# Optimization experiments

Measured on AMD Instinct MI355X. Metric: run time of the kernel, lower is better.

## Reference

```python
import jax, jax.numpy as jnp
import numpy as np

B, S, D = 4, 2048, 1024


def setup_inputs() -> dict:
    key = jax.random.key(0)
    ks = jax.random.split(key, 9)
    scale = 1.0 / np.sqrt(D)
    x = jax.random.normal(ks[0], (B, S, D), dtype=jnp.float32)
    mask = jnp.tril(jnp.ones((S, S), dtype=jnp.int32))[None, :, :]  # causal, broadcast over batch
    Wq = jax.random.normal(ks[1], (D, D), dtype=jnp.float32) * scale
    bq = jax.random.normal(ks[2], (D,), dtype=jnp.float32) * 0.01
    Wk = jax.random.normal(ks[3], (D, D), dtype=jnp.float32) * scale
    bk = jax.random.normal(ks[4], (D,), dtype=jnp.float32) * 0.01
    Wv = jax.random.normal(ks[5], (D, D), dtype=jnp.float32) * scale
    bv = jax.random.normal(ks[6], (D,), dtype=jnp.float32) * 0.01
    Wo = jax.random.normal(ks[7], (D, D), dtype=jnp.float32) * scale
    bo = jax.random.normal(ks[8], (D,), dtype=jnp.float32) * 0.01
    return {"x": x, "mask": mask, "Wq": Wq, "bq": bq, "Wk": Wk, "bk": bk,
            "Wv": Wv, "bv": bv, "Wo": Wo, "bo": bo}


def reference(x, mask, Wq, bq, Wk, bk, Wv, bv, Wo, bo):
    # Linear projections (torch Linear: x @ W^T + b; here W stored as [in, out])
    Q = jnp.einsum('bsd,de->bse', x, Wq) + bq
    K = jnp.einsum('bsd,de->bse', x, Wk) + bk
    V = jnp.einsum('bsd,de->bse', x, Wv) + bv
    d_k = Q.shape[-1]
    scores = jnp.einsum('bqd,bkd->bqk', Q, K) / jnp.sqrt(jnp.float32(d_k))
    scores = jnp.where(mask == 0, jnp.float32(-jnp.inf), scores)
    attn_weights = jax.nn.softmax(scores, axis=-1)  # [B, S, S]
    attn_output = jnp.einsum('bqk,bkd->bqd', attn_weights, V)
    output = jnp.einsum('bsd,de->bse', attn_output, Wo) + bo
    return output, attn_weights
```

## Files before the change

kernel.cpp:

```cpp
#include <hip/hip_runtime.h>
#include <cstdint>
#include <cstddef>
#include <cmath>

typedef __bf16 bf16_t;
typedef bf16_t bf16x8 __attribute__((ext_vector_type(8)));
typedef bf16_t bf16x4 __attribute__((ext_vector_type(4)));
typedef float f32x4 __attribute__((ext_vector_type(4)));

constexpr int kB = 4;
constexpr int kS = 2048;
constexpr int kD = 1024;
constexpr int BM = 128, BN = 128, BK = 32;
constexpr int TILE_ELEMS = (BM + BN) * BK;

typedef __attribute__((address_space(1))) void as1void;
typedef __attribute__((address_space(3))) void as3void;

__device__ __forceinline__ void gload16(const void* g, void* l) {
  __builtin_amdgcn_global_load_lds((as1void*)g, (as3void*)l, 16, 0, 0);
}

__device__ __forceinline__ void gemm_mainloop(
    const bf16_t* __restrict__ A, int lda,
    const bf16_t* __restrict__ B, int ldb,
    int ksteps, bf16_t* lds, f32x4 acc[4][4]) {
  const int tid = threadIdx.x;
  const int w = tid >> 6, lane = tid & 63;
  const int srow = lane >> 2;
  const int scol = (lane & 3) << 3;
  const int wr = (w >> 1) << 6, wc = (w & 1) << 6;
  const int fr = lane & 15, kg = lane >> 4;

  const bf16_t* ga0 = A + (size_t)(w * 16 + srow) * lda + scol;
  const bf16_t* ga1 = A + (size_t)(64 + w * 16 + srow) * lda + scol;
  const bf16_t* gb0 = B + (size_t)(w * 16 + srow) * ldb + scol;
  const bf16_t* gb1 = B + (size_t)(64 + w * 16 + srow) * ldb + scol;
  const int oa0 = (w * 16) * BK;
  const int oa1 = (64 + w * 16) * BK;
  const int ob0 = BM * BK + (w * 16) * BK;
  const int ob1 = BM * BK + (64 + w * 16) * BK;

  gload16(ga0, lds + oa0);
  gload16(ga1, lds + oa1);
  gload16(gb0, lds + ob0);
  gload16(gb1, lds + ob1);
  ga0 += BK; ga1 += BK; gb0 += BK; gb1 += BK;
  __syncthreads();

  int cur = 0;
  for (int ks = 0; ks < ksteps; ++ks) {
    const int nxt = cur ^ 1;
    if (ks + 1 < ksteps) {
      bf16_t* nb = lds + nxt * TILE_ELEMS;
      gload16(ga0, nb + oa0);
      gload16(ga1, nb + oa1);
      gload16(gb0, nb + ob0);
      gload16(gb1, nb + ob1);
      ga0 += BK; ga1 += BK; gb0 += BK; gb1 += BK;
    }
    const bf16_t* cb = lds + cur * TILE_ELEMS;
    bf16x8 af[4], bfv[4];
#pragma unroll
    for (int m = 0; m < 4; ++m)
      af[m] = *(const bf16x8*)(cb + (wr + m * 16 + fr) * BK + kg * 8);
#pragma unroll
    for (int n = 0; n < 4; ++n)
      bfv[n] = *(const bf16x8*)(cb + BM * BK + (wc + n * 16 + fr) * BK + kg * 8);
#pragma unroll
    for (int m = 0; m < 4; ++m)
#pragma unroll
      for (int n = 0; n < 4; ++n)
        acc[m][n] = __builtin_amdgcn_mfma_f32_16x16x32_bf16(af[m], bfv[n],
                                                            acc[m][n], 0, 0, 0);
    __syncthreads();
    cur = nxt;
  }
}


__global__ __launch_bounds__(256)
void k_gemm_qkv(const bf16_t* __restrict__ A, const bf16_t* __restrict__ WT,
                const float* __restrict__ bq, const float* __restrict__ bk,
                const float* __restrict__ bv, bf16_t* __restrict__ Out) {
  __shared__ bf16_t lds[2 * TILE_ELEMS];
  const int which = blockIdx.x >> 3;
  const int n0 = (blockIdx.x & 7) * BN;
  const int m0 = blockIdx.y * BM;
  f32x4 acc[4][4] = {};
  gemm_mainloop(A + (size_t)m0 * kD, kD,
                WT + (size_t)which * kD * kD + (size_t)n0 * kD, kD,
                kD / BK, lds, acc);
  const float* bias = which == 0 ? bq : which == 1 ? bk : bv;
  const int tid = threadIdx.x, w = tid >> 6, lane = tid & 63;
  const int wr = (w >> 1) << 6, wc = (w & 1) << 6, fr = lane & 15, kg = lane >> 4;
  if (which < 2) {
    bf16_t* C = Out + (size_t)which * kB * kS * kD;
#pragma unroll
    for (int n = 0; n < 4; ++n) {
      const int col = n0 + wc + n * 16 + fr;
      const float bvv = bias[col];
#pragma unroll
      for (int m = 0; m < 4; ++m)
#pragma unroll
        for (int i = 0; i < 4; ++i) {
          const int row = m0 + wr + m * 16 + kg * 4 + i;
          C[(size_t)row * kD + col] = (bf16_t)(acc[m][n][i] + bvv);
        }
    }
  } else {
    bf16_t* VT = Out + (size_t)2 * kB * kS * kD;
#pragma unroll
    for (int n = 0; n < 4; ++n) {
      const int col = n0 + wc + n * 16 + fr;
      const float bvv = bias[col];
#pragma unroll
      for (int m = 0; m < 4; ++m)
#pragma unroll
        for (int i = 0; i < 4; ++i) {
          const int row = m0 + wr + m * 16 + kg * 4 + i;
          const int b = row >> 11, s = row & (kS - 1);
          VT[((size_t)b * kD + col) * kS + s] = (bf16_t)(acc[m][n][i] + bvv);
        }
    }
  }
}

__global__ __launch_bounds__(256)
void k_gemm_scores(const bf16_t* __restrict__ Q, const bf16_t* __restrict__ K,
                   float* __restrict__ Sc) {
  const int t = blockIdx.x, b = blockIdx.y;
  int by = (int)((sqrtf(8.f * t + 1.f) - 1.f) * 0.5f);
  while ((by + 1) * (by + 2) / 2 <= t) ++by;
  while (by * (by + 1) / 2 > t) --by;
  const int bx = t - by * (by + 1) / 2;
  __shared__ bf16_t lds[2 * TILE_ELEMS];
  const int m0 = by * BM, n0 = bx * BN;
  f32x4 acc[4][4] = {};
  gemm_mainloop(Q + (size_t)b * kS * kD + (size_t)m0 * kD, kD,
                K + (size_t)b * kS * kD + (size_t)n0 * kD, kD, kD / BK, lds, acc);
  float* Sb = Sc + (size_t)b * kS * kS;
  const int tid = threadIdx.x, w = tid >> 6, lane = tid & 63;
  const int wr = (w >> 1) << 6, wc = (w & 1) << 6, fr = lane & 15, kg = lane >> 4;
#pragma unroll
  for (int m = 0; m < 4; ++m)
#pragma unroll
    for (int n = 0; n < 4; ++n)
#pragma unroll
      for (int i = 0; i < 4; ++i) {
        const int row = m0 + wr + m * 16 + kg * 4 + i;
        const int col = n0 + wc + n * 16 + fr;
        Sb[(size_t)row * kS + col] = acc[m][n][i] * 0.03125f;
      }
}

__global__ __launch_bounds__(256)
void k_softmax(float* __restrict__ P, bf16_t* __restrict__ Pb) {
  const int row = blockIdx.x;
  const int q = row & (kS - 1);
  float* p = P + (size_t)row * kS;
  bf16_t* pb = Pb + (size_t)row * kS;
  const int L = q + 1;
  __shared__ float buf[kS];
  __shared__ float red[8];
  const int tid = threadIdx.x;
  float4* b4 = (float4*)buf;
  const float4* p4 = (const float4*)p;
  b4[tid] = p4[tid];
  b4[tid + 256] = p4[tid + 256];
  __syncthreads();
  float mx = -1e30f;
  for (int k = tid; k < L; k += 256) mx = fmaxf(mx, buf[k]);
#pragma unroll
  for (int s2 = 32; s2 >= 1; s2 >>= 1) mx = fmaxf(mx, __shfl_xor(mx, s2));
  if ((tid & 63) == 0) red[tid >> 6] = mx;
  __syncthreads();
  mx = fmaxf(fmaxf(red[0], red[1]), fmaxf(red[2], red[3]));
  float sm = 0.f;
  for (int k = tid; k < L; k += 256) {
    const float e = __expf(buf[k] - mx);
    buf[k] = e;
    sm += e;
  }
#pragma unroll
  for (int s2 = 32; s2 >= 1; s2 >>= 1) sm += __shfl_xor(sm, s2);
  if ((tid & 63) == 0) red[4 + (tid >> 6)] = sm;
  __syncthreads();
  const float inv = 1.f / (red[4] + red[5] + red[6] + red[7]);
  for (int k = tid; k < L; k += 256) {
    const float v = buf[k] * inv;
    p[k] = v;
    pb[k] = (bf16_t)v;
  }
  for (int k = L + tid; k < kS; k += 256) {
    p[k] = 0.f;
    pb[k] = (bf16_t)0.f;
  }
}

__global__ __launch_bounds__(256)
void k_gemm_pv(const bf16_t* __restrict__ P, const bf16_t* __restrict__ VT,
               bf16_t* __restrict__ AO) {
  const int bx = blockIdx.x, b = blockIdx.z;
  const int by = (int)gridDim.y - 1 - (int)blockIdx.y;
  __shared__ bf16_t lds[2 * TILE_ELEMS];
  const int m0 = by * BM, n0 = bx * BN;
  const int ksteps = (m0 + BM) / BK;
  f32x4 acc[4][4] = {};
  gemm_mainloop(P + (size_t)b * kS * kS + (size_t)m0 * kS, kS,
                VT + (size_t)b * kD * kS + (size_t)n0 * kS, kS, ksteps, lds, acc);
  bf16_t* AOb = AO + (size_t)b * kS * kD;
  const int tid = threadIdx.x, w = tid >> 6, lane = tid & 63;
  const int wr = (w >> 1) << 6, wc = (w & 1) << 6, fr = lane & 15, kg = lane >> 4;
#pragma unroll
  for (int m = 0; m < 4; ++m)
#pragma unroll
    for (int n = 0; n < 4; ++n)
#pragma unroll
      for (int i = 0; i < 4; ++i) {
        const int row = m0 + wr + m * 16 + kg * 4 + i;
        const int col = n0 + wc + n * 16 + fr;
        AOb[(size_t)row * kD + col] = (bf16_t)acc[m][n][i];
      }
}

__global__ __launch_bounds__(256)
void k_gemm_out(const bf16_t* __restrict__ A, const bf16_t* __restrict__ Bw,
                const float* __restrict__ bias, float* __restrict__ C) {
  __shared__ bf16_t lds[2 * TILE_ELEMS];
  const int m0 = blockIdx.y * BM, n0 = blockIdx.x * BN;
  f32x4 acc[4][4] = {};
  gemm_mainloop(A + (size_t)m0 * kD, kD, Bw + (size_t)n0 * kD, kD, kD / BK, lds, acc);
  const int tid = threadIdx.x, w = tid >> 6, lane = tid & 63;
  const int wr = (w >> 1) << 6, wc = (w & 1) << 6, fr = lane & 15, kg = lane >> 4;
#pragma unroll
  for (int n = 0; n < 4; ++n) {
    const int col = n0 + wc + n * 16 + fr;
    const float bv = bias[col];
#pragma unroll
    for (int m = 0; m < 4; ++m)
#pragma unroll
      for (int i = 0; i < 4; ++i) {
        const int row = m0 + wr + m * 16 + kg * 4 + i;
        C[(size_t)row * kD + col] = acc[m][n][i] + bv;
      }
  }
}

__global__ __launch_bounds__(256)
void k_cvt(const float* __restrict__ X, bf16_t* __restrict__ Y, size_t n4) {
  size_t i = (size_t)blockIdx.x * 256 + threadIdx.x;
  const size_t stride = (size_t)gridDim.x * 256;
  const float4* X4 = (const float4*)X;
  bf16x4* Y4 = (bf16x4*)Y;
  for (; i < n4; i += stride) {
    const float4 v = X4[i];
    bf16x4 o = {(bf16_t)v.x, (bf16_t)v.y, (bf16_t)v.z, (bf16_t)v.w};
    Y4[i] = o;
  }
}

__global__ __launch_bounds__(256)
void k_prep_w(const float* __restrict__ W0, const float* __restrict__ W1,
              const float* __restrict__ W2, const float* __restrict__ W3,
              bf16_t* __restrict__ T0, bf16_t* __restrict__ T1,
              bf16_t* __restrict__ T2, bf16_t* __restrict__ T3) {
  const float* W = blockIdx.z == 0 ? W0 : blockIdx.z == 1 ? W1 : blockIdx.z == 2 ? W2 : W3;
  bf16_t* T = blockIdx.z == 0 ? T0 : blockIdx.z == 1 ? T1 : blockIdx.z == 2 ? T2 : T3;
  __shared__ float t[32][33];
  const int tx = threadIdx.x, ty = threadIdx.y;
  const int x0 = blockIdx.x * 32, y0 = blockIdx.y * 32;
#pragma unroll
  for (int j = 0; j < 4; ++j)
    t[ty + 8 * j][tx] = W[(size_t)(y0 + ty + 8 * j) * kD + x0 + tx];
  __syncthreads();
#pragma unroll
  for (int j = 0; j < 4; ++j)
    T[(size_t)(x0 + ty + 8 * j) * kD + y0 + tx] = (bf16_t)t[tx][ty + 8 * j];
}

extern "C" void kernel_launch(void* const* d_in, const int* in_sizes, int n_in,
                              void* d_out, int out_size, void* d_ws, size_t ws_size,
                              hipStream_t stream) {
  (void)in_sizes; (void)n_in; (void)out_size; (void)ws_size;
  const float* x  = (const float*)d_in[0];
  const float* Wq = (const float*)d_in[2];
  const float* bq = (const float*)d_in[3];
  const float* Wk = (const float*)d_in[4];
  const float* bk = (const float*)d_in[5];
  const float* Wv = (const float*)d_in[6];
  const float* bv = (const float*)d_in[7];
  const float* Wo = (const float*)d_in[8];
  const float* bo = (const float*)d_in[9];

  float* out  = (float*)d_out;
  float* Pout = out + (size_t)kB * kS * kD;

  bf16_t* WqT = (bf16_t*)d_ws;
  bf16_t* WkT = WqT + (size_t)kD * kD;
  bf16_t* WvT = WkT + (size_t)kD * kD;
  bf16_t* WoT = WvT + (size_t)kD * kD;
  bf16_t* Qb  = WoT + (size_t)kD * kD;
  bf16_t* Kb  = Qb + (size_t)kB * kS * kD;
  bf16_t* VTb = Kb + (size_t)kB * kS * kD;
  bf16_t* Pb  = VTb + (size_t)kB * kS * kD;
  bf16_t* AOb = Pb + (size_t)kB * kS * kS;
  bf16_t* xb  = AOb + (size_t)kB * kS * kD;

  k_cvt<<<2048, 256, 0, stream>>>(x, xb, (size_t)kB * kS * kD / 4);
  k_prep_w<<<dim3(32, 32, 4), dim3(32, 8), 0, stream>>>(Wq, Wk, Wv, Wo, WqT, WkT, WvT, WoT);
  k_gemm_qkv<<<dim3(24, kB * kS / BM), 256, 0, stream>>>(xb, WqT, bq, bk, bv, Qb);
  k_gemm_scores<<<dim3(136, kB), 256, 0, stream>>>(Qb, Kb, Pout);
  k_softmax<<<kB * kS, 256, 0, stream>>>(Pout, Pb);
  k_gemm_pv<<<dim3(kD / BN, kS / BM, kB), 256, 0, stream>>>(Pb, VTb, AOb);
  k_gemm_out<<<dim3(kD / BN, kB * kS / BM), 256, 0, stream>>>(AOb, WoT, bo, out);
}
```

Before: 232.1 us.

## Template GEMM mainloop with fragment-ordered LDS layout, larger QKV tiles and swizzled grids

Replaces the shared GEMM mainloop with a templated version whose LDS tile layout is stored in MFMA fragment order (16-row groups by k-chunk), which aims to cut LDS bank conflicts on fragment reads. The QKV projection moves to 256x128 tiles with 512 threads, and the QKV and output GEMMs get block-index swizzles for better L2 reuse. The input conversion and weight transpose kernels are merged into one launch, occupancy hints are added, and softmax skips loading masked-out score chunks. Together these aim to raise MFMA throughput and trim launch and memory overhead. The cost is higher register and LDS pressure per block.

Result: slower. 273.1 us (+17.7%).

```diff
diff --git a/kernel.cpp b/kernel.cpp
--- a/kernel.cpp
+++ b/kernel.cpp
@@ -11,8 +11,6 @@
 constexpr int kB = 4;
 constexpr int kS = 2048;
 constexpr int kD = 1024;
-constexpr int BM = 128, BN = 128, BK = 32;
-constexpr int TILE_ELEMS = (BM + BN) * BK;
 
 typedef __attribute__((address_space(1))) void as1void;
 typedef __attribute__((address_space(3))) void as3void;
@@ -21,90 +19,102 @@
   __builtin_amdgcn_global_load_lds((as1void*)g, (as3void*)l, 16, 0, 0);
 }
 
-__device__ __forceinline__ void gemm_mainloop(
+template <int TM, int TN, int NTHR>
+__device__ __forceinline__ void gemm2ph(
     const bf16_t* __restrict__ A, int lda,
     const bf16_t* __restrict__ B, int ldb,
-    int ksteps, bf16_t* lds, f32x4 acc[4][4]) {
+    int nk, bf16_t* lds, f32x4 acc[4][4]) {
+  constexpr int WND = TN / 64;
+  constexpr int IA = TM * 4 / NTHR;
+  constexpr int IB = TN * 4 / NTHR;
+  constexpr int BUF = (TM + TN) * 32;
   const int tid = threadIdx.x;
-  const int w = tid >> 6, lane = tid & 63;
-  const int srow = lane >> 2;
-  const int scol = (lane & 3) << 3;
-  const int wr = (w >> 1) << 6, wc = (w & 1) << 6;
+  const int wid = tid >> 6, lane = tid & 63;
+  const int wm = wid / WND, wn = wid % WND;
   const int fr = lane & 15, kg = lane >> 4;
 
-  const bf16_t* ga0 = A + (size_t)(w * 16 + srow) * lda + scol;
-  const bf16_t* ga1 = A + (size_t)(64 + w * 16 + srow) * lda + scol;
-  const bf16_t* gb0 = B + (size_t)(w * 16 + srow) * ldb + scol;
-  const bf16_t* gb1 = B + (size_t)(64 + w * 16 + srow) * ldb + scol;
-  const int oa0 = (w * 16) * BK;
-  const int oa1 = (64 + w * 16) * BK;
-  const int ob0 = BM * BK + (w * 16) * BK;
-  const int ob1 = BM * BK + (64 + w * 16) * BK;
-
-  gload16(ga0, lds + oa0);
-  gload16(ga1, lds + oa1);
-  gload16(gb0, lds + ob0);
-  gload16(gb1, lds + ob1);
-  ga0 += BK; ga1 += BK; gb0 += BK; gb1 += BK;
+  const bf16_t* gA[IA]; int oA[IA];
+#pragma unroll
+  for (int i = 0; i < IA; ++i) {
+    const int u = tid + i * NTHR;
+    const int r = ((u >> 6) << 4) | (u & 15);
+    const int c = ((u >> 4) & 3) << 3;
+    gA[i] = A + (size_t)r * lda + c;
+    oA[i] = u * 8;
+  }
+  const bf16_t* gB[IB]; int oB[IB];
+#pragma unroll
+  for (int i = 0; i < IB; ++i) {
+    const int u = tid + i * NTHR;
+    const int r = ((u >> 6) << 4) | (u & 15);
+    const int c = ((u >> 4) & 3) << 3;
+    gB[i] = B + (size_t)r * ldb + c;
+    oB[i] = TM * 32 + u * 8;
+  }
+#pragma unroll
+  for (int i = 0; i < IA; ++i) gload16(gA[i], lds + oA[i]);
+#pragma unroll
+  for (int i = 0; i < IB; ++i) gload16(gB[i], lds + oB[i]);
   __syncthreads();
 
   int cur = 0;
-  for (int ks = 0; ks < ksteps; ++ks) {
-    const int nxt = cur ^ 1;
-    if (ks + 1 < ksteps) {
-      bf16_t* nb = lds + nxt * TILE_ELEMS;
-      gload16(ga0, nb + oa0);
-      gload16(ga1, nb + oa1);
-      gload16(gb0, nb + ob0);
-      gload16(gb1, nb + ob1);
-      ga0 += BK; ga1 += BK; gb0 += BK; gb1 += BK;
+  const int aoff = kg * 128 + fr * 8;
+  for (int t = 0; t < nk; ++t) {
+    if (t + 1 < nk) {
+      bf16_t* nb = lds + (cur ^ 1) * BUF;
+#pragma unroll
+      for (int i = 0; i < IA; ++i) gload16(gA[i] + (t + 1) * 32, nb + oA[i]);
+#pragma unroll
+      for (int i = 0; i < IB; ++i) gload16(gB[i] + (t + 1) * 32, nb + oB[i]);
     }
-    const bf16_t* cb = lds + cur * TILE_ELEMS;
-    bf16x8 af[4], bfv[4];
-#pragma unroll
-    for (int m = 0; m < 4; ++m)
-      af[m] = *(const bf16x8*)(cb + (wr + m * 16 + fr) * BK + kg * 8);
+    const bf16_t* cb = lds + cur * BUF;
+    bf16x8 aF[4], bF[4];
+#pragma unroll
+    for (int m = 0; m < 4; ++m)
+      aF[m] = *(const bf16x8*)(cb + (wm * 4 + m) * 512 + aoff);
 #pragma unroll
     for (int n = 0; n < 4; ++n)
-      bfv[n] = *(const bf16x8*)(cb + BM * BK + (wc + n * 16 + fr) * BK + kg * 8);
+      bF[n] = *(const bf16x8*)(cb + TM * 32 + (wn * 4 + n) * 512 + aoff);
 #pragma unroll
     for (int m = 0; m < 4; ++m)
 #pragma unroll
       for (int n = 0; n < 4; ++n)
-        acc[m][n] = __builtin_amdgcn_mfma_f32_16x16x32_bf16(af[m], bfv[n],
+        acc[m][n] = __builtin_amdgcn_mfma_f32_16x16x32_bf16(aF[m], bF[n],
                                                             acc[m][n], 0, 0, 0);
     __syncthreads();
-    cur = nxt;
-  }
-}
-
-
-__global__ __launch_bounds__(256)
-void k_gemm_qkv(const bf16_t* __restrict__ A, const bf16_t* __restrict__ WT,
-                const float* __restrict__ bq, const float* __restrict__ bk,
-                const float* __restrict__ bv, bf16_t* __restrict__ Out) {
-  __shared__ bf16_t lds[2 * TILE_ELEMS];
-  const int which = blockIdx.x >> 3;
-  const int n0 = (blockIdx.x & 7) * BN;
-  const int m0 = blockIdx.y * BM;
+    cur ^= 1;
+  }
+}
+
+
+__global__ __launch_bounds__(512, 4)
+void k_qkv(const bf16_t* __restrict__ A, const bf16_t* __restrict__ WT,
+           const float* __restrict__ bq, const float* __restrict__ bk,
+           const float* __restrict__ bv, bf16_t* __restrict__ Out) {
+  __shared__ bf16_t lds[2 * (256 + 128) * 32];
+  const int id = blockIdx.x;
+  const int swz = (id & 7) * 96 + (id >> 3);
+  const int mb = swz / 24, nbb = swz % 24;
+  const int which = nbb >> 3;
+  const int m0 = mb * 256, n0 = (nbb & 7) * 128;
   f32x4 acc[4][4] = {};
-  gemm_mainloop(A + (size_t)m0 * kD, kD,
-                WT + (size_t)which * kD * kD + (size_t)n0 * kD, kD,
-                kD / BK, lds, acc);
+  gemm2ph<256, 128, 512>(A + (size_t)m0 * kD, kD,
+                         WT + (size_t)which * kD * kD + (size_t)n0 * kD, kD,
+                         kD / 32, lds, acc);
   const float* bias = which == 0 ? bq : which == 1 ? bk : bv;
-  const int tid = threadIdx.x, w = tid >> 6, lane = tid & 63;
-  const int wr = (w >> 1) << 6, wc = (w & 1) << 6, fr = lane & 15, kg = lane >> 4;
+  const int lane = threadIdx.x & 63, wid = threadIdx.x >> 6;
+  const int wm = wid >> 1, wn = wid & 1, fr = lane & 15, kgr = lane >> 4;
   if (which < 2) {
     bf16_t* C = Out + (size_t)which * kB * kS * kD;
 #pragma unroll
     for (int n = 0; n < 4; ++n) {
-      const int col = n0 + wc + n * 16 + fr;
+      const int col = n0 + wn * 64 + n * 16 + fr;
       const float bvv = bias[col];
 #pragma unroll
       for (int m = 0; m < 4; ++m)
 #pragma unroll
         for (int i = 0; i < 4; ++i) {
-          const int row = m0 + wr + m * 16 + kg * 4 + i;
+          const int row = m0 + wm * 64 + m * 16 + kgr * 4 + i;
           C[(size_t)row * kD + col] = (bf16_t)(acc[m][n][i] + bvv);
         }
     }
@@ -112,13 +122,13 @@
     bf16_t* VT = Out + (size_t)2 * kB * kS * kD;
 #pragma unroll
     for (int n = 0; n < 4; ++n) {
-      const int col = n0 + wc + n * 16 + fr;
+      const int col = n0 + wn * 64 + n * 16 + fr;
       const float bvv = bias[col];
 #pragma unroll
       for (int m = 0; m < 4; ++m)
 #pragma unroll
         for (int i = 0; i < 4; ++i) {
-          const int row = m0 + wr + m * 16 + kg * 4 + i;
+          const int row = m0 + wm * 64 + m * 16 + kgr * 4 + i;
           const int b = row >> 11, s = row & (kS - 1);
           VT[((size_t)b * kD + col) * kS + s] = (bf16_t)(acc[m][n][i] + bvv);
         }
@@ -126,32 +136,88 @@
   }
 }
 
-__global__ __launch_bounds__(256)
-void k_gemm_scores(const bf16_t* __restrict__ Q, const bf16_t* __restrict__ K,
-                   float* __restrict__ Sc) {
+__global__ __launch_bounds__(256, 4)
+void k_scores(const bf16_t* __restrict__ Q, const bf16_t* __restrict__ K,
+              float* __restrict__ Sc) {
   const int t = blockIdx.x, b = blockIdx.y;
   int by = (int)((sqrtf(8.f * t + 1.f) - 1.f) * 0.5f);
   while ((by + 1) * (by + 2) / 2 <= t) ++by;
   while (by * (by + 1) / 2 > t) --by;
   const int bx = t - by * (by + 1) / 2;
-  __shared__ bf16_t lds[2 * TILE_ELEMS];
-  const int m0 = by * BM, n0 = bx * BN;
+  __shared__ bf16_t lds[2 * 256 * 32];
+  const int m0 = by * 128, n0 = bx * 128;
   f32x4 acc[4][4] = {};
-  gemm_mainloop(Q + (size_t)b * kS * kD + (size_t)m0 * kD, kD,
-                K + (size_t)b * kS * kD + (size_t)n0 * kD, kD, kD / BK, lds, acc);
+  gemm2ph<128, 128, 256>(Q + (size_t)b * kS * kD + (size_t)m0 * kD, kD,
+                         K + (size_t)b * kS * kD + (size_t)n0 * kD, kD,
+                         kD / 32, lds, acc);
   float* Sb = Sc + (size_t)b * kS * kS;
-  const int tid = threadIdx.x, w = tid >> 6, lane = tid & 63;
-  const int wr = (w >> 1) << 6, wc = (w & 1) << 6, fr = lane & 15, kg = lane >> 4;
-#pragma unroll
-  for (int m = 0; m < 4; ++m)
-#pragma unroll
-    for (int n = 0; n < 4; ++n)
+  const int lane = threadIdx.x & 63, wid = threadIdx.x >> 6;
+  const int wm = wid >> 1, wn = wid & 1, fr = lane & 15, kgr = lane >> 4;
+#pragma unroll
+  for (int n = 0; n < 4; ++n) {
+    const int col = n0 + wn * 64 + n * 16 + fr;
+#pragma unroll
+    for (int m = 0; m < 4; ++m)
 #pragma unroll
       for (int i = 0; i < 4; ++i) {
-        const int row = m0 + wr + m * 16 + kg * 4 + i;
-        const int col = n0 + wc + n * 16 + fr;
+        const int row = m0 + wm * 64 + m * 16 + kgr * 4 + i;
         Sb[(size_t)row * kS + col] = acc[m][n][i] * 0.03125f;
       }
+  }
+}
+
+__global__ __launch_bounds__(256, 4)
+void k_pv(const bf16_t* __restrict__ P, const bf16_t* __restrict__ VT,
+          bf16_t* __restrict__ AO) {
+  const int bx = blockIdx.x, b = blockIdx.z;
+  const int by = (int)gridDim.y - 1 - (int)blockIdx.y;
+  __shared__ bf16_t lds[2 * 256 * 32];
+  const int m0 = by * 128, n0 = bx * 128;
+  const int nk = (m0 + 128) / 32;
+  f32x4 acc[4][4] = {};
+  gemm2ph<128, 128, 256>(P + (size_t)b * kS * kS + (size_t)m0 * kS, kS,
+                         VT + (size_t)b * kD * kS + (size_t)n0 * kS, kS,
+                         nk, lds, acc);
+  bf16_t* AOb = AO + (size_t)b * kS * kD;
+  const int lane = threadIdx.x & 63, wid = threadIdx.x >> 6;
+  const int wm = wid >> 1, wn = wid & 1, fr = lane & 15, kgr = lane >> 4;
+#pragma unroll
+  for (int n = 0; n < 4; ++n) {
+    const int col = n0 + wn * 64 + n * 16 + fr;
+#pragma unroll
+    for (int m = 0; m < 4; ++m)
+#pragma unroll
+      for (int i = 0; i < 4; ++i) {
+        const int row = m0 + wm * 64 + m * 16 + kgr * 4 + i;
+        AOb[(size_t)row * kD + col] = (bf16_t)acc[m][n][i];
+      }
+  }
+}
+
+__global__ __launch_bounds__(256, 4)
+void k_out(const bf16_t* __restrict__ A, const bf16_t* __restrict__ Bw,
+           const float* __restrict__ bias, float* __restrict__ C) {
+  __shared__ bf16_t lds[2 * 256 * 32];
+  const int id = blockIdx.x;
+  const int swz = (id & 7) * 64 + (id >> 3);
+  const int m0 = (swz >> 3) * 128, n0 = (swz & 7) * 128;
+  f32x4 acc[4][4] = {};
+  gemm2ph<128, 128, 256>(A + (size_t)m0 * kD, kD, Bw + (size_t)n0 * kD, kD,
+                         kD / 32, lds, acc);
+  const int lane = threadIdx.x & 63, wid = threadIdx.x >> 6;
+  const int wm = wid >> 1, wn = wid & 1, fr = lane & 15, kgr = lane >> 4;
+#pragma unroll
+  for (int n = 0; n < 4; ++n) {
+    const int col = n0 + wn * 64 + n * 16 + fr;
+    const float bvv = bias[col];
+#pragma unroll
+    for (int m = 0; m < 4; ++m)
+#pragma unroll
+      for (int i = 0; i < 4; ++i) {
+        const int row = m0 + wm * 64 + m * 16 + kgr * 4 + i;
+        C[(size_t)row * kD + col] = acc[m][n][i] + bvv;
+      }
+  }
 }
 
 __global__ __launch_bounds__(256)
@@ -166,8 +232,8 @@
   const int tid = threadIdx.x;
   float4* b4 = (float4*)buf;
   const float4* p4 = (const float4*)p;
-  b4[tid] = p4[tid];
-  b4[tid + 256] = p4[tid + 256];
+  if (tid * 4 < L) b4[tid] = p4[tid];
+  if (1024 + tid * 4 < L) b4[tid + 256] = p4[tid + 256];
   __syncthreads();
   float mx = -1e30f;
   for (int k = tid; k < L; k += 256) mx = fmaxf(mx, buf[k]);
@@ -199,76 +265,28 @@
 }
 
 __global__ __launch_bounds__(256)
-void k_gemm_pv(const bf16_t* __restrict__ P, const bf16_t* __restrict__ VT,
-               bf16_t* __restrict__ AO) {
-  const int bx = blockIdx.x, b = blockIdx.z;
-  const int by = (int)gridDim.y - 1 - (int)blockIdx.y;
-  __shared__ bf16_t lds[2 * TILE_ELEMS];
-  const int m0 = by * BM, n0 = bx * BN;
-  const int ksteps = (m0 + BM) / BK;
-  f32x4 acc[4][4] = {};
-  gemm_mainloop(P + (size_t)b * kS * kS + (size_t)m0 * kS, kS,
-                VT + (size_t)b * kD * kS + (size_t)n0 * kS, kS, ksteps, lds, acc);
-  bf16_t* AOb = AO + (size_t)b * kS * kD;
-  const int tid = threadIdx.x, w = tid >> 6, lane = tid & 63;
-  const int wr = (w >> 1) << 6, wc = (w & 1) << 6, fr = lane & 15, kg = lane >> 4;
-#pragma unroll
-  for (int m = 0; m < 4; ++m)
-#pragma unroll
-    for (int n = 0; n < 4; ++n)
-#pragma unroll
-      for (int i = 0; i < 4; ++i) {
-        const int row = m0 + wr + m * 16 + kg * 4 + i;
-        const int col = n0 + wc + n * 16 + fr;
-        AOb[(size_t)row * kD + col] = (bf16_t)acc[m][n][i];
-      }
-}
-
-__global__ __launch_bounds__(256)
-void k_gemm_out(const bf16_t* __restrict__ A, const bf16_t* __restrict__ Bw,
-                const float* __restrict__ bias, float* __restrict__ C) {
-  __shared__ bf16_t lds[2 * TILE_ELEMS];
-  const int m0 = blockIdx.y * BM, n0 = blockIdx.x * BN;
-  f32x4 acc[4][4] = {};
-  gemm_mainloop(A + (size_t)m0 * kD, kD, Bw + (size_t)n0 * kD, kD, kD / BK, lds, acc);
-  const int tid = threadIdx.x, w = tid >> 6, lane = tid & 63;
-  const int wr = (w >> 1) << 6, wc = (w & 1) << 6, fr = lane & 15, kg = lane >> 4;
-#pragma unroll
-  for (int n = 0; n < 4; ++n) {
-    const int col = n0 + wc + n * 16 + fr;
-    const float bv = bias[col];
-#pragma unroll
-    for (int m = 0; m < 4; ++m)
-#pragma unroll
-      for (int i = 0; i < 4; ++i) {
-        const int row = m0 + wr + m * 16 + kg * 4 + i;
-        C[(size_t)row * kD + col] = acc[m][n][i] + bv;
-      }
-  }
-}
-
-__global__ __launch_bounds__(256)
-void k_cvt(const float* __restrict__ X, bf16_t* __restrict__ Y, size_t n4) {
-  size_t i = (size_t)blockIdx.x * 256 + threadIdx.x;
-  const size_t stride = (size_t)gridDim.x * 256;
-  const float4* X4 = (const float4*)X;
-  bf16x4* Y4 = (bf16x4*)Y;
-  for (; i < n4; i += stride) {
-    const float4 v = X4[i];
-    bf16x4 o = {(bf16_t)v.x, (bf16_t)v.y, (bf16_t)v.z, (bf16_t)v.w};
-    Y4[i] = o;
-  }
-}
-
-__global__ __launch_bounds__(256)
-void k_prep_w(const float* __restrict__ W0, const float* __restrict__ W1,
-              const float* __restrict__ W2, const float* __restrict__ W3,
-              bf16_t* __restrict__ T0, bf16_t* __restrict__ T1,
-              bf16_t* __restrict__ T2, bf16_t* __restrict__ T3) {
+void k_prep(const float* __restrict__ X, bf16_t* __restrict__ Y,
+            const float* __restrict__ W0, const float* __restrict__ W1,
+            const float* __restrict__ W2, const float* __restrict__ W3,
+            bf16_t* __restrict__ T0, bf16_t* __restrict__ T1,
+            bf16_t* __restrict__ T2, bf16_t* __restrict__ T3) {
+  const int tx = threadIdx.x & 31, ty = threadIdx.x >> 5;
+  if (blockIdx.z == 4) {
+    const size_t n4 = (size_t)kB * kS * kD / 4;
+    size_t i = ((size_t)blockIdx.y * 32 + blockIdx.x) * 256 + threadIdx.x;
+    const size_t stride = (size_t)1024 * 256;
+    const float4* X4 = (const float4*)X;
+    bf16x4* Y4 = (bf16x4*)Y;
+    for (; i < n4; i += stride) {
+      const float4 v = X4[i];
+      bf16x4 o = {(bf16_t)v.x, (bf16_t)v.y, (bf16_t)v.z, (bf16_t)v.w};
+      Y4[i] = o;
+    }
+    return;
+  }
   const float* W = blockIdx.z == 0 ? W0 : blockIdx.z == 1 ? W1 : blockIdx.z == 2 ? W2 : W3;
   bf16_t* T = blockIdx.z == 0 ? T0 : blockIdx.z == 1 ? T1 : blockIdx.z == 2 ? T2 : T3;
   __shared__ float t[32][33];
-  const int tx = threadIdx.x, ty = threadIdx.y;
   const int x0 = blockIdx.x * 32, y0 = blockIdx.y * 32;
 #pragma unroll
   for (int j = 0; j < 4; ++j)
@@ -307,11 +325,11 @@
   bf16_t* AOb = Pb + (size_t)kB * kS * kS;
   bf16_t* xb  = AOb + (size_t)kB * kS * kD;
 
-  k_cvt<<<2048, 256, 0, stream>>>(x, xb, (size_t)kB * kS * kD / 4);
-  k_prep_w<<<dim3(32, 32, 4), dim3(32, 8), 0, stream>>>(Wq, Wk, Wv, Wo, WqT, WkT, WvT, WoT);
-  k_gemm_qkv<<<dim3(24, kB * kS / BM), 256, 0, stream>>>(xb, WqT, bq, bk, bv, Qb);
-  k_gemm_scores<<<dim3(136, kB), 256, 0, stream>>>(Qb, Kb, Pout);
+  k_prep<<<dim3(32, 32, 5), 256, 0, stream>>>(x, xb, Wq, Wk, Wv, Wo,
+                                              WqT, WkT, WvT, WoT);
+  k_qkv<<<768, 512, 0, stream>>>(xb, WqT, bq, bk, bv, Qb);
+  k_scores<<<dim3(136, kB), 256, 0, stream>>>(Qb, Kb, Pout);
   k_softmax<<<kB * kS, 256, 0, stream>>>(Pout, Pb);
-  k_gemm_pv<<<dim3(kD / BN, kS / BM, kB), 256, 0, stream>>>(Pb, VTb, AOb);
-  k_gemm_out<<<dim3(kD / BN, kB * kS / BM), 256, 0, stream>>>(AOb, WoT, bo, out);
-}
+  k_pv<<<dim3(8, 16, kB), 256, 0, stream>>>(Pb, VTb, AOb);
+  k_out<<<512, 256, 0, stream>>>(AOb, WoT, bo, out);
+}
```

## Use 8-wave phased pipelined QKV GEMM, fuse prep kernels, trim softmax loads

Applied to the files above, without the earlier changes.

Replaces the QKV projection GEMM with a 512-thread, 128x256-tile kernel. Each K-step is split into four phases, with global-to-LDS loads interleaved between MFMA groups, explicit waitcnt and barriers, s_setprio around the MFMAs, and a swizzled block ordering. It also merges the x conversion and weight transpose into one launch, and makes softmax skip loading fully masked float4 chunks of each row. The hand-scheduled pipeline aims to hide load latency and reduce launch overhead, at the cost of fragile manual synchronisation and higher LDS use per block.

Result: no change. 234.2 us (+0.9%).

```diff
diff --git a/kernel.cpp b/kernel.cpp
--- a/kernel.cpp
+++ b/kernel.cpp
@@ -19,6 +19,12 @@
 
 __device__ __forceinline__ void gload16(const void* g, void* l) {
   __builtin_amdgcn_global_load_lds((as1void*)g, (as3void*)l, 16, 0, 0);
+}
+
+__device__ __forceinline__ void wgbar() {
+  asm volatile("" ::: "memory");
+  __builtin_amdgcn_s_barrier();
+  asm volatile("" ::: "memory");
 }
 
 __device__ __forceinline__ void gemm_mainloop(
@@ -78,33 +84,137 @@
   }
 }
 
-
-__global__ __launch_bounds__(256)
-void k_gemm_qkv(const bf16_t* __restrict__ A, const bf16_t* __restrict__ WT,
-                const float* __restrict__ bq, const float* __restrict__ bk,
-                const float* __restrict__ bv, bf16_t* __restrict__ Out) {
-  __shared__ bf16_t lds[2 * TILE_ELEMS];
-  const int which = blockIdx.x >> 3;
-  const int n0 = (blockIdx.x & 7) * BN;
-  const int m0 = blockIdx.y * BM;
+__device__ __forceinline__ void gemm8ph(
+    const bf16_t* __restrict__ A, int lda,
+    const bf16_t* __restrict__ B, int ldb,
+    int nk, bf16_t* lds, f32x4 acc[4][4]) {
+  const int tid = threadIdx.x;
+  const int wid = tid >> 6, lane = tid & 63;
+  const int wm = wid >> 2, wn = wid & 3;
+  const int fr = lane & 15, kg = (lane >> 4) & 3;
+  const int srow = ((tid >> 7) << 4) | (tid & 15);
+  const int scol = ((tid >> 4) & 7) << 3;
+  const bf16_t* pA = A + (size_t)srow * lda + scol;
+  const bf16_t* pB = B + (size_t)srow * ldb + scol;
+  const int dst = tid * 8;
+
+  auto stgA = [&](int t, int j) {
+    gload16(pA + (size_t)(j * 64) * lda + t * 64,
+            lds + (t & 1) * 24576 + j * 4096 + dst);
+  };
+  auto stgB = [&](int t, int j) {
+    gload16(pB + (size_t)(j * 64) * ldb + t * 64,
+            lds + (t & 1) * 24576 + 8192 + j * 4096 + dst);
+  };
+
+  stgB(0, 0); stgB(0, 1); stgB(0, 2); stgB(0, 3);
+  stgA(0, 0); stgA(0, 1);
+  if (nk > 1) {
+    stgB(1, 0); stgB(1, 1); stgB(1, 2); stgB(1, 3);
+    asm volatile("s_waitcnt vmcnt(4)" ::: "memory");
+  } else {
+    asm volatile("s_waitcnt vmcnt(0)" ::: "memory");
+  }
+  wgbar();
+
+  const int ro = kg * 128 + fr * 8;
+  for (int t = 0; t < nk; ++t) {
+    const bf16_t* bb = lds + (t & 1) * 24576;
+    const bf16_t* as = bb + wm * 4096;
+    const bf16_t* bs = bb + 8192 + wn * 4096;
+    bf16x8 bF[4][2], aF[2];
+#pragma unroll
+    for (int n = 0; n < 4; ++n) {
+      bF[n][0] = *(const bf16x8*)(bs + n * 1024 + ro);
+      bF[n][1] = *(const bf16x8*)(bs + n * 1024 + 512 + ro);
+    }
+    aF[0] = *(const bf16x8*)(as + ro);
+    aF[1] = *(const bf16x8*)(as + 512 + ro);
+    if (t + 1 < nk) { stgA(t + 1, 0); stgA(t + 1, 1); }
+    wgbar();
+    __builtin_amdgcn_s_setprio(1);
+#pragma unroll
+    for (int n = 0; n < 4; ++n) {
+      acc[0][n] = __builtin_amdgcn_mfma_f32_16x16x32_bf16(aF[0], bF[n][0], acc[0][n], 0, 0, 0);
+      acc[0][n] = __builtin_amdgcn_mfma_f32_16x16x32_bf16(aF[1], bF[n][1], acc[0][n], 0, 0, 0);
+    }
+    __builtin_amdgcn_s_setprio(0);
+    asm volatile("s_waitcnt lgkmcnt(0)" ::: "memory");
+    wgbar();
+    aF[0] = *(const bf16x8*)(as + 1024 + ro);
+    aF[1] = *(const bf16x8*)(as + 1024 + 512 + ro);
+    if (t + 2 < nk) { stgB(t + 2, 0); stgB(t + 2, 1); }
+    wgbar();
+    __builtin_amdgcn_s_setprio(1);
+#pragma unroll
+    for (int n = 0; n < 4; ++n) {
+      acc[1][n] = __builtin_amdgcn_mfma_f32_16x16x32_bf16(aF[0], bF[n][0], acc[1][n], 0, 0, 0);
+      acc[1][n] = __builtin_amdgcn_mfma_f32_16x16x32_bf16(aF[1], bF[n][1], acc[1][n], 0, 0, 0);
+    }
+    __builtin_amdgcn_s_setprio(0);
+    asm volatile("s_waitcnt lgkmcnt(0)" ::: "memory");
+    wgbar();
+    aF[0] = *(const bf16x8*)(as + 2048 + ro);
+    aF[1] = *(const bf16x8*)(as + 2048 + 512 + ro);
+    if (t + 2 < nk) { stgB(t + 2, 2); stgB(t + 2, 3); }
+    wgbar();
+    __builtin_amdgcn_s_setprio(1);
+#pragma unroll
+    for (int n = 0; n < 4; ++n) {
+      acc[2][n] = __builtin_amdgcn_mfma_f32_16x16x32_bf16(aF[0], bF[n][0], acc[2][n], 0, 0, 0);
+      acc[2][n] = __builtin_amdgcn_mfma_f32_16x16x32_bf16(aF[1], bF[n][1], acc[2][n], 0, 0, 0);
+    }
+    __builtin_amdgcn_s_setprio(0);
+    asm volatile("s_waitcnt lgkmcnt(0)" ::: "memory");
+    wgbar();
+    aF[0] = *(const bf16x8*)(as + 3072 + ro);
+    aF[1] = *(const bf16x8*)(as + 3072 + 512 + ro);
+    wgbar();
+    __builtin_amdgcn_s_setprio(1);
+#pragma unroll
+    for (int n = 0; n < 4; ++n) {
+      acc[3][n] = __builtin_amdgcn_mfma_f32_16x16x32_bf16(aF[0], bF[n][0], acc[3][n], 0, 0, 0);
+      acc[3][n] = __builtin_amdgcn_mfma_f32_16x16x32_bf16(aF[1], bF[n][1], acc[3][n], 0, 0, 0);
+    }
+    __builtin_amdgcn_s_setprio(0);
+    asm volatile("s_waitcnt lgkmcnt(0)" ::: "memory");
+    if (t < nk - 1) {
+      if (t + 2 < nk) asm volatile("s_waitcnt vmcnt(4)" ::: "memory");
+      else            asm volatile("s_waitcnt vmcnt(0)" ::: "memory");
+    }
+    wgbar();
+  }
+}
+
+
+__global__ __launch_bounds__(512)
+void k_qkv8(const bf16_t* __restrict__ A, const bf16_t* __restrict__ WT,
+            const float* __restrict__ bq, const float* __restrict__ bk,
+            const float* __restrict__ bv, bf16_t* __restrict__ Out) {
+  __shared__ bf16_t lds[49152];
+  const int id = blockIdx.x;
+  const int swz = (id & 7) * 96 + (id >> 3);
+  const int mb = swz / 12, nb = swz % 12;
+  const int which = nb >> 2;
+  const int m0 = mb * 128, n0 = (nb & 3) * 256;
   f32x4 acc[4][4] = {};
-  gemm_mainloop(A + (size_t)m0 * kD, kD,
-                WT + (size_t)which * kD * kD + (size_t)n0 * kD, kD,
-                kD / BK, lds, acc);
+  gemm8ph(A + (size_t)m0 * kD, kD,
+          WT + (size_t)which * kD * kD + (size_t)n0 * kD, kD,
+          kD / 64, lds, acc);
   const float* bias = which == 0 ? bq : which == 1 ? bk : bv;
-  const int tid = threadIdx.x, w = tid >> 6, lane = tid & 63;
-  const int wr = (w >> 1) << 6, wc = (w & 1) << 6, fr = lane & 15, kg = lane >> 4;
+  const int lane = threadIdx.x & 63, wid = threadIdx.x >> 6;
+  const int wm = wid >> 2, wn = wid & 3, fr = lane & 15, kgr = lane >> 4;
   if (which < 2) {
     bf16_t* C = Out + (size_t)which * kB * kS * kD;
 #pragma unroll
     for (int n = 0; n < 4; ++n) {
-      const int col = n0 + wc + n * 16 + fr;
+      const int col = n0 + wn * 64 + n * 16 + fr;
       const float bvv = bias[col];
 #pragma unroll
       for (int m = 0; m < 4; ++m)
 #pragma unroll
         for (int i = 0; i < 4; ++i) {
-          const int row = m0 + wr + m * 16 + kg * 4 + i;
+          const int row = m0 + wm * 64 + m * 16 + kgr * 4 + i;
           C[(size_t)row * kD + col] = (bf16_t)(acc[m][n][i] + bvv);
         }
     }
@@ -112,13 +222,13 @@
     bf16_t* VT = Out + (size_t)2 * kB * kS * kD;
 #pragma unroll
     for (int n = 0; n < 4; ++n) {
-      const int col = n0 + wc + n * 16 + fr;
+      const int col = n0 + wn * 64 + n * 16 + fr;
       const float bvv = bias[col];
 #pragma unroll
       for (int m = 0; m < 4; ++m)
 #pragma unroll
         for (int i = 0; i < 4; ++i) {
-          const int row = m0 + wr + m * 16 + kg * 4 + i;
+          const int row = m0 + wm * 64 + m * 16 + kgr * 4 + i;
           const int b = row >> 11, s = row & (kS - 1);
           VT[((size_t)b * kD + col) * kS + s] = (bf16_t)(acc[m][n][i] + bvv);
         }
@@ -166,8 +276,8 @@
   const int tid = threadIdx.x;
   float4* b4 = (float4*)buf;
   const float4* p4 = (const float4*)p;
-  b4[tid] = p4[tid];
-  b4[tid + 256] = p4[tid + 256];
+  if (tid * 4 < L) b4[tid] = p4[tid];
+  if (1024 + tid * 4 < L) b4[tid + 256] = p4[tid + 256];
   __syncthreads();
   float mx = -1e30f;
   for (int k = tid; k < L; k += 256) mx = fmaxf(mx, buf[k]);
@@ -248,27 +358,28 @@
 }
 
 __global__ __launch_bounds__(256)
-void k_cvt(const float* __restrict__ X, bf16_t* __restrict__ Y, size_t n4) {
-  size_t i = (size_t)blockIdx.x * 256 + threadIdx.x;
-  const size_t stride = (size_t)gridDim.x * 256;
-  const float4* X4 = (const float4*)X;
-  bf16x4* Y4 = (bf16x4*)Y;
-  for (; i < n4; i += stride) {
-    const float4 v = X4[i];
-    bf16x4 o = {(bf16_t)v.x, (bf16_t)v.y, (bf16_t)v.z, (bf16_t)v.w};
-    Y4[i] = o;
-  }
-}
-
-__global__ __launch_bounds__(256)
-void k_prep_w(const float* __restrict__ W0, const float* __restrict__ W1,
-              const float* __restrict__ W2, const float* __restrict__ W3,
-              bf16_t* __restrict__ T0, bf16_t* __restrict__ T1,
-              bf16_t* __restrict__ T2, bf16_t* __restrict__ T3) {
+void k_prep(const float* __restrict__ X, bf16_t* __restrict__ Y,
+            const float* __restrict__ W0, const float* __restrict__ W1,
+            const float* __restrict__ W2, const float* __restrict__ W3,
+            bf16_t* __restrict__ T0, bf16_t* __restrict__ T1,
+            bf16_t* __restrict__ T2, bf16_t* __restrict__ T3) {
+  const int tx = threadIdx.x & 31, ty = threadIdx.x >> 5;
+  if (blockIdx.z == 4) {
+    const size_t n4 = (size_t)kB * kS * kD / 4;
+    size_t i = ((size_t)blockIdx.y * 32 + blockIdx.x) * 256 + threadIdx.x;
+    const size_t stride = (size_t)1024 * 256;
+    const float4* X4 = (const float4*)X;
+    bf16x4* Y4 = (bf16x4*)Y;
+    for (; i < n4; i += stride) {
+      const float4 v = X4[i];
+      bf16x4 o = {(bf16_t)v.x, (bf16_t)v.y, (bf16_t)v.z, (bf16_t)v.w};
+      Y4[i] = o;
+    }
+    return;
+  }
   const float* W = blockIdx.z == 0 ? W0 : blockIdx.z == 1 ? W1 : blockIdx.z == 2 ? W2 : W3;
   bf16_t* T = blockIdx.z == 0 ? T0 : blockIdx.z == 1 ? T1 : blockIdx.z == 2 ? T2 : T3;
   __shared__ float t[32][33];
-  const int tx = threadIdx.x, ty = threadIdx.y;
   const int x0 = blockIdx.x * 32, y0 = blockIdx.y * 32;
 #pragma unroll
   for (int j = 0; j < 4; ++j)
@@ -307,11 +418,11 @@
   bf16_t* AOb = Pb + (size_t)kB * kS * kS;
   bf16_t* xb  = AOb + (size_t)kB * kS * kD;
 
-  k_cvt<<<2048, 256, 0, stream>>>(x, xb, (size_t)kB * kS * kD / 4);
-  k_prep_w<<<dim3(32, 32, 4), dim3(32, 8), 0, stream>>>(Wq, Wk, Wv, Wo, WqT, WkT, WvT, WoT);
-  k_gemm_qkv<<<dim3(24, kB * kS / BM), 256, 0, stream>>>(xb, WqT, bq, bk, bv, Qb);
+  k_prep<<<dim3(32, 32, 5), 256, 0, stream>>>(x, xb, Wq, Wk, Wv, Wo,
+                                              WqT, WkT, WvT, WoT);
+  k_qkv8<<<768, 512, 0, stream>>>(xb, WqT, bq, bk, bv, Qb);
   k_gemm_scores<<<dim3(136, kB), 256, 0, stream>>>(Qb, Kb, Pout);
   k_softmax<<<kB * kS, 256, 0, stream>>>(Pout, Pb);
-  k_gemm_pv<<<dim3(kD / BN, kS / BM, kB), 256, 0, stream>>>(Pb, VTb, AOb);
-  k_gemm_out<<<dim3(kD / BN, kB * kS / BM), 256, 0, stream>>>(AOb, WoT, bo, out);
-}
+  k_gemm_pv<<<dim3(8, 16, kB), 256, 0, stream>>>(Pb, VTb, AOb);
+  k_gemm_out<<<dim3(8, 64), 256, 0, stream>>>(AOb, WoT, bo, out);
+}
```

## Add 256x256 ping-pong GEMM for Q/K projection, fuse prep kernels, swizzle tiles

Applied to the files above, without the earlier changes.

Splits the QKV projection into a new 512-thread 256x256-tile GEMM for Q and K, with a multi-stage global-to-LDS pipeline, interleaved staging, raw barriers and setprio. V keeps the 128-tile path and moves to its own kernel. It also fuses the x conversion and weight transpose into one launch, adds block-index swizzling to the V and output GEMMs, and makes softmax load only the causal prefix of each row. The aim is higher MFMA utilisation and better L2 reuse, at the cost of heavier register and LDS pressure and fragile hand-written waitcnt logic.

New measurement: 220.9 us. 1.05x faster.

```diff
diff --git a/kernel.cpp b/kernel.cpp
--- a/kernel.cpp
+++ b/kernel.cpp
@@ -19,6 +19,12 @@
 
 __device__ __forceinline__ void gload16(const void* g, void* l) {
   __builtin_amdgcn_global_load_lds((as1void*)g, (as3void*)l, 16, 0, 0);
+}
+
+__device__ __forceinline__ void wgbar() {
+  asm volatile("" ::: "memory");
+  __builtin_amdgcn_s_barrier();
+  asm volatile("" ::: "memory");
 }
 
 __device__ __forceinline__ void gemm_mainloop(
@@ -78,51 +84,137 @@
   }
 }
 
-
-__global__ __launch_bounds__(256)
-void k_gemm_qkv(const bf16_t* __restrict__ A, const bf16_t* __restrict__ WT,
-                const float* __restrict__ bq, const float* __restrict__ bk,
-                const float* __restrict__ bv, bf16_t* __restrict__ Out) {
+__device__ __forceinline__ void gemm256_loop(
+    const bf16_t* __restrict__ A, int lda,
+    const bf16_t* __restrict__ B, int ldb,
+    int nk, bf16_t* lds, f32x4 acc[8][4]) {
+  const int tid = threadIdx.x;
+  const int wid = tid >> 6, lane = tid & 63;
+  const int wm = wid >> 2, wn = wid & 3;
+  const int fr = lane & 15, kg = (lane >> 4) & 3;
+  const int s_row = ((tid >> 7) << 4) | (tid & 15);
+  const int s_col = ((tid >> 4) & 7) << 3;
+  const bf16_t* pA = A + (size_t)s_row * lda + s_col;
+  const bf16_t* pB = B + (size_t)s_row * ldb + s_col;
+  const int ldst = wid << 9;
+
+  auto stg = [&](int tt, int op, int h, int j) {
+    const bf16_t* g = (op ? pB : pA) + (size_t)(h * 128 + j * 64) * (op ? ldb : lda)
+                      + (size_t)tt * 64;
+    bf16_t* d = lds + (((tt & 1) * 4 + op * 2 + h) * 8192) + j * 4096 + ldst;
+    gload16(g, d);
+  };
+
+#pragma unroll
+  for (int h = 0; h < 2; ++h)
+#pragma unroll
+    for (int j = 0; j < 2; ++j) { stg(0, 0, h, j); stg(0, 1, h, j); }
+  stg(1, 1, 0, 0); stg(1, 1, 0, 1); stg(1, 1, 1, 0); stg(1, 1, 1, 1);
+  stg(1, 0, 0, 0); stg(1, 0, 1, 0);
+  asm volatile("s_waitcnt vmcnt(6)" ::: "memory");
+  wgbar();
+
+  const int arow = kg * 128 + fr * 8;
+  for (int t = 0; t < nk; ++t) {
+    const bf16_t* sb = lds + (t & 1) * 32768;
+    const bf16_t* aslot = sb + wm * 8192;
+    const bf16_t* bslot = sb + (2 + (wn >> 1)) * 8192 + (wn & 1) * 4096;
+    bf16x8 bF[4][2];
+#pragma unroll
+    for (int q = 0; q < 4; ++q) {
+      bf16x8 aF[2][2];
+#pragma unroll
+      for (int mi = 0; mi < 2; ++mi)
+#pragma unroll
+        for (int ks = 0; ks < 2; ++ks)
+          aF[mi][ks] = *(const bf16x8*)(aslot + (2 * q + mi) * 1024 + ks * 512 + arow);
+      if (q == 0) {
+#pragma unroll
+        for (int n = 0; n < 4; ++n)
+#pragma unroll
+          for (int ks = 0; ks < 2; ++ks)
+            bF[n][ks] = *(const bf16x8*)(bslot + n * 1024 + ks * 512 + arow);
+      }
+      if (q == 0)      { if (t + 1 <= nk - 1) { stg(t + 1, 0, 0, 1); stg(t + 1, 0, 1, 1); } }
+      else if (q == 1) { if (t + 2 <= nk - 1) { stg(t + 2, 1, 0, 0); stg(t + 2, 1, 0, 1); } }
+      else if (q == 2) { if (t + 2 <= nk - 1) { stg(t + 2, 1, 1, 0); stg(t + 2, 1, 1, 1); } }
+      else             { if (t + 2 <= nk - 1) { stg(t + 2, 0, 0, 0); stg(t + 2, 0, 1, 0); } }
+      wgbar();
+      __builtin_amdgcn_s_setprio(1);
+#pragma unroll
+      for (int mi = 0; mi < 2; ++mi)
+#pragma unroll
+        for (int n = 0; n < 4; ++n)
+#pragma unroll
+          for (int ks = 0; ks < 2; ++ks)
+            acc[2 * q + mi][n] = __builtin_amdgcn_mfma_f32_16x16x32_bf16(
+                aF[mi][ks], bF[n][ks], acc[2 * q + mi][n], 0, 0, 0);
+      __builtin_amdgcn_s_setprio(0);
+      asm volatile("s_waitcnt lgkmcnt(0)" ::: "memory");
+      if (q == 3 && t < nk - 1) {
+        if (t + 2 <= nk - 1) asm volatile("s_waitcnt vmcnt(6)" ::: "memory");
+        else                 asm volatile("s_waitcnt vmcnt(0)" ::: "memory");
+      }
+      wgbar();
+    }
+  }
+}
+
+
+__global__ __launch_bounds__(512, 2)
+void k_qk256(const bf16_t* __restrict__ A, const bf16_t* __restrict__ WT,
+             const float* __restrict__ bq, const float* __restrict__ bk,
+             bf16_t* __restrict__ Qb, bf16_t* __restrict__ Kb) {
+  __shared__ bf16_t lds[65536];
+  const int id = blockIdx.x;
+  const int swz = (id & 7) * 32 + (id >> 3);
+  const int mb = swz >> 3, nb = swz & 7;
+  const int m0 = mb * 256, n0 = nb * 256;
+  f32x4 acc[8][4] = {};
+  gemm256_loop(A + (size_t)m0 * kD, kD, WT + (size_t)n0 * kD, kD,
+               kD / 64, lds, acc);
+  const int lane = threadIdx.x & 63, wid = threadIdx.x >> 6;
+  const int wm = wid >> 2, wn = wid & 3, fr = lane & 15, kgr = lane >> 4;
+  const int which = n0 >> 10;
+  bf16_t* C = which == 0 ? Qb : Kb;
+  const float* bias = which == 0 ? bq : bk;
+#pragma unroll
+  for (int n = 0; n < 4; ++n) {
+    const int col = (n0 & 1023) + wn * 64 + n * 16 + fr;
+    const float bvv = bias[col];
+#pragma unroll
+    for (int m = 0; m < 8; ++m)
+#pragma unroll
+      for (int i = 0; i < 4; ++i) {
+        const int row = m0 + wm * 128 + m * 16 + kgr * 4 + i;
+        C[(size_t)row * kD + col] = (bf16_t)(acc[m][n][i] + bvv);
+      }
+  }
+}
+
+__global__ __launch_bounds__(256)
+void k_v128(const bf16_t* __restrict__ A, const bf16_t* __restrict__ Bw,
+            const float* __restrict__ bias, bf16_t* __restrict__ VT) {
   __shared__ bf16_t lds[2 * TILE_ELEMS];
-  const int which = blockIdx.x >> 3;
-  const int n0 = (blockIdx.x & 7) * BN;
-  const int m0 = blockIdx.y * BM;
+  const int id = blockIdx.x;
+  const int swz = (id & 7) * 64 + (id >> 3);
+  const int m0 = (swz >> 3) * BM, n0 = (swz & 7) * BN;
   f32x4 acc[4][4] = {};
-  gemm_mainloop(A + (size_t)m0 * kD, kD,
-                WT + (size_t)which * kD * kD + (size_t)n0 * kD, kD,
-                kD / BK, lds, acc);
-  const float* bias = which == 0 ? bq : which == 1 ? bk : bv;
+  gemm_mainloop(A + (size_t)m0 * kD, kD, Bw + (size_t)n0 * kD, kD, kD / BK, lds, acc);
   const int tid = threadIdx.x, w = tid >> 6, lane = tid & 63;
   const int wr = (w >> 1) << 6, wc = (w & 1) << 6, fr = lane & 15, kg = lane >> 4;
-  if (which < 2) {
-    bf16_t* C = Out + (size_t)which * kB * kS * kD;
-#pragma unroll
-    for (int n = 0; n < 4; ++n) {
-      const int col = n0 + wc + n * 16 + fr;
-      const float bvv = bias[col];
-#pragma unroll
-      for (int m = 0; m < 4; ++m)
-#pragma unroll
-        for (int i = 0; i < 4; ++i) {
-          const int row = m0 + wr + m * 16 + kg * 4 + i;
-          C[(size_t)row * kD + col] = (bf16_t)(acc[m][n][i] + bvv);
-        }
-    }
-  } else {
-    bf16_t* VT = Out + (size_t)2 * kB * kS * kD;
-#pragma unroll
-    for (int n = 0; n < 4; ++n) {
-      const int col = n0 + wc + n * 16 + fr;
-      const float bvv = bias[col];
-#pragma unroll
-      for (int m = 0; m < 4; ++m)
-#pragma unroll
-        for (int i = 0; i < 4; ++i) {
-          const int row = m0 + wr + m * 16 + kg * 4 + i;
-          const int b = row >> 11, s = row & (kS - 1);
-          VT[((size_t)b * kD + col) * kS + s] = (bf16_t)(acc[m][n][i] + bvv);
-        }
-    }
+#pragma unroll
+  for (int n = 0; n < 4; ++n) {
+    const int col = n0 + wc + n * 16 + fr;
+    const float bvv = bias[col];
+#pragma unroll
+    for (int m = 0; m < 4; ++m)
+#pragma unroll
+      for (int i = 0; i < 4; ++i) {
+        const int row = m0 + wr + m * 16 + kg * 4 + i;
+        const int b = row >> 11, s = row & (kS - 1);
+        VT[((size_t)b * kD + col) * kS + s] = (bf16_t)(acc[m][n][i] + bvv);
+      }
   }
 }
 
@@ -166,8 +258,8 @@
   const int tid = threadIdx.x;
   float4* b4 = (float4*)buf;
   const float4* p4 = (const float4*)p;
-  b4[tid] = p4[tid];
-  b4[tid + 256] = p4[tid + 256];
+  if (tid * 4 < L) b4[tid] = p4[tid];
+  if (1024 + tid * 4 < L) b4[tid + 256] = p4[tid + 256];
   __syncthreads();
   float mx = -1e30f;
   for (int k = tid; k < L; k += 256) mx = fmaxf(mx, buf[k]);
@@ -228,7 +320,9 @@
 void k_gemm_out(const bf16_t* __restrict__ A, const bf16_t* __restrict__ Bw,
                 const float* __restrict__ bias, float* __restrict__ C) {
   __shared__ bf16_t lds[2 * TILE_ELEMS];
-  const int m0 = blockIdx.y * BM, n0 = blockIdx.x * BN;
+  const int id = blockIdx.x;
+  const int swz = (id & 7) * 64 + (id >> 3);
+  const int m0 = (swz >> 3) * BM, n0 = (swz & 7) * BN;
   f32x4 acc[4][4] = {};
   gemm_mainloop(A + (size_t)m0 * kD, kD, Bw + (size_t)n0 * kD, kD, kD / BK, lds, acc);
   const int tid = threadIdx.x, w = tid >> 6, lane = tid & 63;
@@ -248,27 +342,28 @@
 }
 
 __global__ __launch_bounds__(256)
-void k_cvt(const float* __restrict__ X, bf16_t* __restrict__ Y, size_t n4) {
-  size_t i = (size_t)blockIdx.x * 256 + threadIdx.x;
-  const size_t stride = (size_t)gridDim.x * 256;
-  const float4* X4 = (const float4*)X;
-  bf16x4* Y4 = (bf16x4*)Y;
-  for (; i < n4; i += stride) {
-    const float4 v = X4[i];
-    bf16x4 o = {(bf16_t)v.x, (bf16_t)v.y, (bf16_t)v.z, (bf16_t)v.w};
-    Y4[i] = o;
-  }
-}
-
-__global__ __launch_bounds__(256)
-void k_prep_w(const float* __restrict__ W0, const float* __restrict__ W1,
-              const float* __restrict__ W2, const float* __restrict__ W3,
-              bf16_t* __restrict__ T0, bf16_t* __restrict__ T1,
-              bf16_t* __restrict__ T2, bf16_t* __restrict__ T3) {
+void k_prep(const float* __restrict__ X, bf16_t* __restrict__ Y,
+            const float* __restrict__ W0, const float* __restrict__ W1,
+            const float* __restrict__ W2, const float* __restrict__ W3,
+            bf16_t* __restrict__ T0, bf16_t* __restrict__ T1,
+            bf16_t* __restrict__ T2, bf16_t* __restrict__ T3) {
+  const int tx = threadIdx.x & 31, ty = threadIdx.x >> 5;
+  if (blockIdx.z == 4) {
+    const size_t n4 = (size_t)kB * kS * kD / 4;
+    size_t i = ((size_t)blockIdx.y * 32 + blockIdx.x) * 256 + threadIdx.x;
+    const size_t stride = (size_t)1024 * 256;
+    const float4* X4 = (const float4*)X;
+    bf16x4* Y4 = (bf16x4*)Y;
+    for (; i < n4; i += stride) {
+      const float4 v = X4[i];
+      bf16x4 o = {(bf16_t)v.x, (bf16_t)v.y, (bf16_t)v.z, (bf16_t)v.w};
+      Y4[i] = o;
+    }
+    return;
+  }
   const float* W = blockIdx.z == 0 ? W0 : blockIdx.z == 1 ? W1 : blockIdx.z == 2 ? W2 : W3;
   bf16_t* T = blockIdx.z == 0 ? T0 : blockIdx.z == 1 ? T1 : blockIdx.z == 2 ? T2 : T3;
   __shared__ float t[32][33];
-  const int tx = threadIdx.x, ty = threadIdx.y;
   const int x0 = blockIdx.x * 32, y0 = blockIdx.y * 32;
 #pragma unroll
   for (int j = 0; j < 4; ++j)
@@ -307,11 +402,12 @@
   bf16_t* AOb = Pb + (size_t)kB * kS * kS;
   bf16_t* xb  = AOb + (size_t)kB * kS * kD;
 
-  k_cvt<<<2048, 256, 0, stream>>>(x, xb, (size_t)kB * kS * kD / 4);
-  k_prep_w<<<dim3(32, 32, 4), dim3(32, 8), 0, stream>>>(Wq, Wk, Wv, Wo, WqT, WkT, WvT, WoT);
-  k_gemm_qkv<<<dim3(24, kB * kS / BM), 256, 0, stream>>>(xb, WqT, bq, bk, bv, Qb);
+  k_prep<<<dim3(32, 32, 5), 256, 0, stream>>>(x, xb, Wq, Wk, Wv, Wo,
+                                              WqT, WkT, WvT, WoT);
+  k_qk256<<<256, 512, 0, stream>>>(xb, WqT, bq, bk, Qb, Kb);
+  k_v128<<<512, 256, 0, stream>>>(xb, WvT, bv, VTb);
   k_gemm_scores<<<dim3(136, kB), 256, 0, stream>>>(Qb, Kb, Pout);
   k_softmax<<<kB * kS, 256, 0, stream>>>(Pout, Pb);
-  k_gemm_pv<<<dim3(kD / BN, kS / BM, kB), 256, 0, stream>>>(Pb, VTb, AOb);
-  k_gemm_out<<<dim3(kD / BN, kB * kS / BM), 256, 0, stream>>>(AOb, WoT, bo, out);
-}
+  k_gemm_pv<<<dim3(8, 16, kB), 256, 0, stream>>>(Pb, VTb, AOb);
+  k_gemm_out<<<512, 256, 0, stream>>>(AOb, WoT, bo, out);
+}
```
